# Kernel tuning notes

Hardware: AMD Instinct MI355X
Metric: run time of the kernel (lower is better)

The kernel has to match this reference:

```python
import jax, jax.numpy as jnp
import numpy as np

B, T, K = 256, 512, 128

def setup_inputs() -> dict:
    key = jax.random.key(0)
    k1, k2, k3, k4, k5 = jax.random.split(key, 5)
    emissions = jax.random.normal(k1, (B, T, K), dtype=jnp.float32)
    tags = jax.random.randint(k2, (B, T), 0, K)
    mask = jnp.ones((B, T), dtype=bool)
    # xavier_uniform_ for trans: limit = sqrt(6/(fan_in+fan_out))
    limit = float(np.sqrt(6.0 / (K + K)))
    trans = jax.random.uniform(k3, (K, K), minval=-limit, maxval=limit, dtype=jnp.float32)
    start = 0.1 * jax.random.normal(k4, (K,), dtype=jnp.float32)
    end = 0.1 * jax.random.normal(k5, (K,), dtype=jnp.float32)
    return {"emissions": emissions, "trans": trans, "start": start, "end": end,
            "tags": tags, "mask": mask}

def reference(emissions, trans, start, end, tags, mask):
    # --- log partition (forward algorithm) via lax.scan over time ---
    em_t = jnp.moveaxis(emissions, 1, 0)  # [T,B,K]
    mk_t = jnp.moveaxis(mask, 1, 0)       # [T,B]
    alpha0 = start + em_t[0]              # [B,K]

    def step(alpha, xs):
        em, mk = xs                                      # em:[B,K], mk:[B]
        scores = alpha[:, :, None] + trans[None] + em[:, None, :]  # [B,K,K]
        alpha_next = jax.nn.logsumexp(scores, axis=1)    # [B,K]
        alpha = jnp.where(mk[:, None], alpha_next, alpha)
        return alpha, None

    alpha, _ = jax.lax.scan(step, alpha0, (em_t[1:], mk_t[1:]))
    logZ = jax.nn.logsumexp(alpha + end, axis=1)  # [B]

    # --- gold path score, fully vectorized ---
    emit = jnp.take_along_axis(emissions, tags[..., None], axis=2)[..., 0]  # [B,T]
    trans_sc = trans[tags[:, :-1], tags[:, 1:]]                             # [B,T-1]
    step_sc = (emit[:, 1:] + trans_sc) * mask[:, 1:]                        # masked steps
    score = start[tags[:, 0]] + emit[:, 0] + jnp.sum(step_sc, axis=1)
    last_idx = jnp.sum(mask, axis=1).astype(jnp.int32) - 1
    last_tags = jnp.take_along_axis(tags, last_idx[:, None], axis=1)[:, 0]
    score = score + end[last_tags]

    return jnp.mean(logZ - score)
```

## Files before the change

kernel.cpp:

```cpp
#include <hip/hip_runtime.h>

#define B_ 256
#define T_ 512
#define K_ 128
#define HALF_T 256

typedef _Float16 half8 __attribute__((ext_vector_type(8)));
typedef _Float16 half2_t __attribute__((ext_vector_type(2)));
typedef float f32x4 __attribute__((ext_vector_type(4)));

__device__ inline float fast_exp2(float x) {
#if __has_builtin(__builtin_amdgcn_exp2f)
    return __builtin_amdgcn_exp2f(x);
#else
    return exp2f(x);
#endif
}
__device__ inline float fast_log2(float x) {
#if __has_builtin(__builtin_amdgcn_logf)
    return __builtin_amdgcn_logf(x);
#else
    return log2f(x);
#endif
}
__device__ inline float dot2(half2_t a, half2_t b, float c) {
#if __has_builtin(__builtin_amdgcn_fdot2)
    return __builtin_amdgcn_fdot2(a, b, c, false);
#else
    return fmaf((float)a.x, (float)b.x, fmaf((float)a.y, (float)b.y, c));
#endif
}
__device__ inline unsigned pack2(float x, float y) {
#if __has_builtin(__builtin_amdgcn_cvt_pkrtz)
    auto h = __builtin_amdgcn_cvt_pkrtz(x, y);
    return __builtin_bit_cast(unsigned, h);
#else
    half2_t h; h.x = (_Float16)x; h.y = (_Float16)y;
    return __builtin_bit_cast(unsigned, h);
#endif
}
__device__ inline half2_t as_h2(unsigned u) {
    return __builtin_bit_cast(half2_t, u);
}

#define WS_TT   0
#define WS_FV   (K_ * K_)
#define WS_BV   (WS_FV + B_ * 64)
#define WS_M2F  (WS_BV + B_ * 64)
#define WS_M2B  (WS_M2F + B_)
#define WS_SCF  (WS_M2B + B_)
#define WS_SCB  (WS_SCF + B_)

__global__ void crf_transpose_kernel(const float* __restrict__ trans,
                                     float* __restrict__ transT)
{
    int idx = blockIdx.x * 256 + threadIdx.x;
    int r = idx >> 7, c = idx & (K_ - 1);
    transT[c * K_ + r] = trans[r * K_ + c];
}


__global__ __launch_bounds__(256, 1)
void crf_half_kernel(const float* __restrict__ emissions,
                     const float* __restrict__ trans,
                     const float* __restrict__ start,
                     const float* __restrict__ endv,
                     const int* __restrict__ tags,
                     unsigned* __restrict__ ws_u32)
{
    const int bid  = blockIdx.x;
    const bool fwd = bid < B_;
    const int b    = fwd ? bid : bid - B_;
    const int tid  = threadIdx.x;
    const int wave = tid >> 6;
    const int lane = tid & 63;
    const int l15  = lane & 15;
    const int g4   = lane >> 4;
    const int colbase = (wave << 5) + l15;

    __shared__ __align__(16) _Float16 emlds[HALF_T][K_];
    __shared__ __align__(16) _Float16 aebuf[2][K_];
    __shared__ float wred[4];

    const float* transT = (const float*)(ws_u32 + WS_TT);
    unsigned*    fv     = ws_u32 + WS_FV;
    unsigned*    bv     = ws_u32 + WS_BV;
    float*       m2f    = (float*)(ws_u32 + WS_M2F);
    float*       m2b    = (float*)(ws_u32 + WS_M2B);
    float*       scf    = (float*)(ws_u32 + WS_SCF);
    float*       scb    = (float*)(ws_u32 + WS_SCB);

    const float L  = 1.44269504f;
    const float C2 = 7.7f;

    const float* M   = fwd ? trans : transT;
    const float* sv_ = fwd ? start : endv;
    const int rbase   = fwd ? 0 : HALF_T;
    const int r0      = fwd ? 0 : (HALF_T - 1);
    const int NIT     = fwd ? (HALF_T - 1) : HALF_T;
    const int em_base = fwd ? 0 : (HALF_T - 1);
    const int em_sign = fwd ? 1 : -1;

    {
        const float4* ef4 = reinterpret_cast<const float4*>(
            emissions + ((size_t)b * T_ + rbase) * K_);
        #pragma unroll
        for (int rd = 0; rd < 2; ++rd) {
            float4 tmp[16];
            #pragma unroll
            for (int u = 0; u < 16; ++u)
                tmp[u] = ef4[(rd * 16 + u) * 256 + tid];
            #pragma unroll
            for (int u = 0; u < 16; ++u) {
                int f = (rd * 16 + u) * 256 + tid;
                int r = f >> 5, m = f & 31;
                uint2 w;
                w.x = pack2(tmp[u].x, tmp[u].y);
                w.y = pack2(tmp[u].z, tmp[u].w);
                *reinterpret_cast<uint2*>(&emlds[r][4 * m]) = w;
            }
        }
    }

#define EFRAG(kc, nc, dst)                                                  \
    {                                                                       \
        half8 t;                                                            \
        _Pragma("unroll")                                                   \
        for (int i = 0; i < 8; ++i) {                                       \
            int k = (kc) * 32 + g4 * 8 + i;                                 \
            t[i] = (_Float16)fast_exp2(M[k * K_ + colbase + 16 * (nc)] * L);\
        }                                                                   \
        dst = t;                                                            \
    }
    half8 e00, e01, e10, e11, e20, e21, e30, e31;
    EFRAG(0, 0, e00) EFRAG(0, 1, e01)
    EFRAG(1, 0, e10) EFRAG(1, 1, e11)
    EFRAG(2, 0, e20) EFRAG(2, 1, e21)
    EFRAG(3, 0, e30) EFRAG(3, 1, e31)
#undef EFRAG

    __syncthreads();

    float M2;
    {
        int ij = tid & 127;
        float z = (sv_[ij] + (float)emlds[r0][ij]) * L;
        float mx = z;
        #pragma unroll
        for (int d = 1; d < 64; d <<= 1) mx = fmaxf(mx, __shfl_xor(mx, d));
        if (lane == 0) wred[wave] = mx;
        __syncthreads();
        M2 = fmaxf(fmaxf(wred[0], wred[1]), fmaxf(wred[2], wred[3]));
        if (tid < K_) aebuf[0][ij] = (_Float16)fast_exp2(z - M2);
    }
    __syncthreads();

    for (int n = 1; n <= NIT; ++n) {
        const _Float16* aerow = aebuf[(n - 1) & 1];

        const char* abase = (const char*)aerow + (g4 << 4);
        half8 a0 = *reinterpret_cast<const half8*>(abase);
        half8 a1 = *reinterpret_cast<const half8*>(abase + 64);
        half8 a2 = *reinterpret_cast<const half8*>(abase + 128);
        half8 a3 = *reinterpret_cast<const half8*>(abase + 192);

        uint2 pr = *reinterpret_cast<const uint2*>(aerow);

        const int emrow = em_base + em_sign * n;
        float em0 = 0.f, em1 = 0.f;
        if (emrow >= 0) {
            em0 = (float)emlds[emrow][colbase];
            em1 = (float)emlds[emrow][colbase + 16];
        }

        f32x4 c0a = {0,0,0,0}, c0b = {0,0,0,0};
        f32x4 c1a = {0,0,0,0}, c1b = {0,0,0,0};
        c0a = __builtin_amdgcn_mfma_f32_16x16x32_f16(a0, e00, c0a, 0, 0, 0);
        c1a = __builtin_amdgcn_mfma_f32_16x16x32_f16(a0, e01, c1a, 0, 0, 0);
        c0b = __builtin_amdgcn_mfma_f32_16x16x32_f16(a1, e10, c0b, 0, 0, 0);
        c1b = __builtin_amdgcn_mfma_f32_16x16x32_f16(a1, e11, c1b, 0, 0, 0);
        c0a = __builtin_amdgcn_mfma_f32_16x16x32_f16(a2, e20, c0a, 0, 0, 0);
        c1a = __builtin_amdgcn_mfma_f32_16x16x32_f16(a2, e21, c1a, 0, 0, 0);
        c0b = __builtin_amdgcn_mfma_f32_16x16x32_f16(a3, e30, c0b, 0, 0, 0);
        c1b = __builtin_amdgcn_mfma_f32_16x16x32_f16(a3, e31, c1b, 0, 0, 0);

        half2_t q0 = as_h2(pr.x), q1 = as_h2(pr.y);
        float pm = fmaxf(fmaxf((float)q0.x, (float)q0.y),
                         fmaxf((float)q1.x, (float)q1.y));
        pm = fmaxf(pm, 6.1e-5f);
        float corr = fast_log2(pm);
        float F0 = fast_exp2(fmaf(em0, L, -C2 - corr));
        float F1 = fast_exp2(fmaf(em1, L, -C2 - corr));

        if (g4 == 0) {
            _Float16* nb = aebuf[n & 1];
            nb[colbase]      = (_Float16)((c0a[0] + c0b[0]) * F0);
            nb[colbase + 16] = (_Float16)((c1a[0] + c1b[0]) * F1);
        }
        M2 += C2 + corr;
        __syncthreads();
    }

    if (tid < 64) {
        unsigned v = *reinterpret_cast<const unsigned*>(&aebuf[NIT & 1][tid * 2]);
        (fwd ? fv : bv)[(size_t)b * 64 + tid] = v;
    }
    if (tid == 0)
        (fwd ? m2f : m2b)[b] = M2;

    {
        const int kk = (fwd ? 0 : HALF_T) + tid;
        const int*   tg  = tags + (size_t)b * T_;
        const float* eb2 = emissions + (size_t)b * T_ * K_;
        int cur = tg[kk];
        float sc = eb2[(size_t)kk * K_ + cur];
        if (kk > 0) sc += trans[tg[kk - 1] * K_ + cur];
        if (fwd && kk == 0) sc += start[cur];
        if (!fwd && kk == T_ - 1) sc += endv[cur];
        #pragma unroll
        for (int d = 1; d < 64; d <<= 1) sc += __shfl_xor(sc, d);
        __syncthreads();
        if (lane == 0) wred[wave] = sc;
        __syncthreads();
        if (tid == 0)
            (fwd ? scf : scb)[b] = wred[0] + wred[1] + wred[2] + wred[3];
    }
}

__global__ void crf_join_kernel(const unsigned* __restrict__ ws_u32,
                                float* __restrict__ out)
{
    const unsigned* fv  = ws_u32 + WS_FV;
    const unsigned* bv  = ws_u32 + WS_BV;
    const float*    m2f = (const float*)(ws_u32 + WS_M2F);
    const float*    m2b = (const float*)(ws_u32 + WS_M2B);
    const float*    scf = (const float*)(ws_u32 + WS_SCF);
    const float*    scb = (const float*)(ws_u32 + WS_SCB);

    const float LN2 = 0.69314718f;
    int b = threadIdx.x;

    float acc = 0.0f;
    #pragma unroll
    for (int k = 0; k < 64; ++k)
        acc = dot2(as_h2(fv[b * 64 + k]), as_h2(bv[b * 64 + k]), acc);

    float logZ = (m2f[b] + m2b[b] + fast_log2(acc)) * LN2;
    float v = logZ - scf[b] - scb[b];

    #pragma unroll
    for (int d = 1; d < 64; d <<= 1) v += __shfl_xor(v, d);
    __shared__ float w[4];
    if ((threadIdx.x & 63) == 0) w[threadIdx.x >> 6] = v;
    __syncthreads();
    if (threadIdx.x == 0)
        out[0] = (w[0] + w[1] + w[2] + w[3]) * (1.0f / 256.0f);
}

extern "C" void kernel_launch(void* const* d_in, const int* in_sizes, int n_in,
                              void* d_out, int out_size, void* d_ws, size_t ws_size,
                              hipStream_t stream)
{
    const float* emissions = (const float*)d_in[0];
    const float* trans     = (const float*)d_in[1];
    const float* start     = (const float*)d_in[2];
    const float* endv      = (const float*)d_in[3];
    const int*   tags      = (const int*)d_in[4];

    unsigned* ws = (unsigned*)d_ws;

    crf_transpose_kernel<<<K_ * K_ / 256, 256, 0, stream>>>(trans, (float*)(ws + WS_TT));
    crf_half_kernel<<<2 * B_, 256, 0, stream>>>(emissions, trans, start, endv, tags, ws);
    crf_join_kernel<<<1, 256, 0, stream>>>(ws, (float*)d_out);
}
```

Before: 108.9 us.

## Stream emissions from global with register prefetch instead of LDS staging

Drops the up-front staging of a half-sequence of emissions into a 64KB LDS buffer. Each step now loads the two needed emission values from global memory through a 4-deep register prefetch pipeline, so latency is hidden behind the recurrence. It also raises wave priority around the MFMA block and replaces __syncthreads with a hand-written lgkmcnt wait plus s_barrier that does not wait on outstanding global loads. This removes the prologue load and conversion and the LDS footprint, but puts a global load on every serial step and keeps emissions in fp32 rather than fp16.

```diff
diff --git a/kernel.cpp b/kernel.cpp
--- a/kernel.cpp
+++ b/kernel.cpp
@@ -28,15 +28,6 @@
     return __builtin_amdgcn_fdot2(a, b, c, false);
 #else
     return fmaf((float)a.x, (float)b.x, fmaf((float)a.y, (float)b.y, c));
-#endif
-}
-__device__ inline unsigned pack2(float x, float y) {
-#if __has_builtin(__builtin_amdgcn_cvt_pkrtz)
-    auto h = __builtin_amdgcn_cvt_pkrtz(x, y);
-    return __builtin_bit_cast(unsigned, h);
-#else
-    half2_t h; h.x = (_Float16)x; h.y = (_Float16)y;
-    return __builtin_bit_cast(unsigned, h);
 #endif
 }
 __device__ inline half2_t as_h2(unsigned u) {
@@ -78,7 +69,6 @@
     const int g4   = lane >> 4;
     const int colbase = (wave << 5) + l15;
 
-    __shared__ __align__(16) _Float16 emlds[HALF_T][K_];
     __shared__ __align__(16) _Float16 aebuf[2][K_];
     __shared__ float wred[4];
 
@@ -101,26 +91,7 @@
     const int em_base = fwd ? 0 : (HALF_T - 1);
     const int em_sign = fwd ? 1 : -1;
 
-    {
-        const float4* ef4 = reinterpret_cast<const float4*>(
-            emissions + ((size_t)b * T_ + rbase) * K_);
-        #pragma unroll
-        for (int rd = 0; rd < 2; ++rd) {
-            float4 tmp[16];
-            #pragma unroll
-            for (int u = 0; u < 16; ++u)
-                tmp[u] = ef4[(rd * 16 + u) * 256 + tid];
-            #pragma unroll
-            for (int u = 0; u < 16; ++u) {
-                int f = (rd * 16 + u) * 256 + tid;
-                int r = f >> 5, m = f & 31;
-                uint2 w;
-                w.x = pack2(tmp[u].x, tmp[u].y);
-                w.y = pack2(tmp[u].z, tmp[u].w);
-                *reinterpret_cast<uint2*>(&emlds[r][4 * m]) = w;
-            }
-        }
-    }
+    const float* emg = emissions + ((size_t)b * T_ + rbase) * K_;
 
 #define EFRAG(kc, nc, dst)                                                  \
     {                                                                       \
@@ -139,12 +110,10 @@
     EFRAG(3, 0, e30) EFRAG(3, 1, e31)
 #undef EFRAG
 
-    __syncthreads();
-
     float M2;
     {
         int ij = tid & 127;
-        float z = (sv_[ij] + (float)emlds[r0][ij]) * L;
+        float z = (sv_[ij] + emg[(size_t)r0 * K_ + ij]) * L;
         float mx = z;
         #pragma unroll
         for (int d = 1; d < 64; d <<= 1) mx = fmaxf(mx, __shfl_xor(mx, d));
@@ -155,8 +124,26 @@
     }
     __syncthreads();
 
+#define EMLOAD(step, va, vb, fl)                                            \
+    {                                                                       \
+        int ern = em_base + em_sign * (step);                               \
+        bool ok = (unsigned)ern <= 255u;                                    \
+        int er  = ok ? ern : 0;                                             \
+        va = emg[(size_t)er * K_ + colbase];                                \
+        vb = emg[(size_t)er * K_ + colbase + 16];                           \
+        fl = ok ? 1.0f : 0.0f;                                              \
+    }
+    float v0a, v0b, f0v, v1a, v1b, f1v, v2a, v2b, f2v, v3a, v3b, f3v;
+    EMLOAD(1, v0a, v0b, f0v)
+    EMLOAD(2, v1a, v1b, f1v)
+    EMLOAD(3, v2a, v2b, f2v)
+    EMLOAD(4, v3a, v3b, f3v)
+
     for (int n = 1; n <= NIT; ++n) {
         const _Float16* aerow = aebuf[(n - 1) & 1];
+
+        float v4a, v4b, f4v;
+        EMLOAD(n + 4, v4a, v4b, f4v)
 
         const char* abase = (const char*)aerow + (g4 << 4);
         half8 a0 = *reinterpret_cast<const half8*>(abase);
@@ -166,15 +153,9 @@
 
         uint2 pr = *reinterpret_cast<const uint2*>(aerow);
 
-        const int emrow = em_base + em_sign * n;
-        float em0 = 0.f, em1 = 0.f;
-        if (emrow >= 0) {
-            em0 = (float)emlds[emrow][colbase];
-            em1 = (float)emlds[emrow][colbase + 16];
-        }
-
         f32x4 c0a = {0,0,0,0}, c0b = {0,0,0,0};
         f32x4 c1a = {0,0,0,0}, c1b = {0,0,0,0};
+        __builtin_amdgcn_s_setprio(1);
         c0a = __builtin_amdgcn_mfma_f32_16x16x32_f16(a0, e00, c0a, 0, 0, 0);
         c1a = __builtin_amdgcn_mfma_f32_16x16x32_f16(a0, e01, c1a, 0, 0, 0);
         c0b = __builtin_amdgcn_mfma_f32_16x16x32_f16(a1, e10, c0b, 0, 0, 0);
@@ -183,14 +164,15 @@
         c1a = __builtin_amdgcn_mfma_f32_16x16x32_f16(a2, e21, c1a, 0, 0, 0);
         c0b = __builtin_amdgcn_mfma_f32_16x16x32_f16(a3, e30, c0b, 0, 0, 0);
         c1b = __builtin_amdgcn_mfma_f32_16x16x32_f16(a3, e31, c1b, 0, 0, 0);
+        __builtin_amdgcn_s_setprio(0);
 
         half2_t q0 = as_h2(pr.x), q1 = as_h2(pr.y);
         float pm = fmaxf(fmaxf((float)q0.x, (float)q0.y),
                          fmaxf((float)q1.x, (float)q1.y));
         pm = fmaxf(pm, 6.1e-5f);
         float corr = fast_log2(pm);
-        float F0 = fast_exp2(fmaf(em0, L, -C2 - corr));
-        float F1 = fast_exp2(fmaf(em1, L, -C2 - corr));
+        float F0 = fast_exp2(fmaf(v0a * f0v, L, -C2 - corr));
+        float F1 = fast_exp2(fmaf(v0b * f0v, L, -C2 - corr));
 
         if (g4 == 0) {
             _Float16* nb = aebuf[n & 1];
@@ -198,8 +180,15 @@
             nb[colbase + 16] = (_Float16)((c1a[0] + c1b[0]) * F1);
         }
         M2 += C2 + corr;
-        __syncthreads();
-    }
+
+        v0a = v1a; v0b = v1b; f0v = f1v;
+        v1a = v2a; v1b = v2b; f1v = f2v;
+        v2a = v3a; v2b = v3b; f2v = f3v;
+        v3a = v4a; v3b = v4b; f3v = f4v;
+
+        asm volatile("s_waitcnt lgkmcnt(0)\n\ts_barrier" ::: "memory");
+    }
+#undef EMLOAD
 
     if (tid < 64) {
         unsigned v = *reinterpret_cast<const unsigned*>(&aebuf[NIT & 1][tid * 2]);
```

Result: slower. 114.8 us (+5.4%).
